# Optimization experiments

Measured on AMD Instinct MI355X. Metric: run time of the kernel, lower is better.

## Reference

```python
import jax, jax.numpy as jnp
import numpy as np
import math

B, I, O, D, H = 32, 1152, 10, 16, 10
SUB = 0.8
S = math.ceil(SUB * I)  # 922 subset size


def _safe_l2norm(x, axis, keepdims=False):
    # L2 norm with zero-safe gradient (forward-identical to jnp.linalg.norm)
    s = jnp.sum(x * x, axis=axis, keepdims=keepdims)
    return jnp.where(s == 0, 0.0, jnp.sqrt(jnp.where(s == 0, 1.0, s)))


def setup_inputs() -> dict:
    key = jax.random.key(0)
    k1, k2 = jax.random.split(key)
    u_predict = jax.random.normal(k1, (B, I, O, D), dtype=jnp.float32)
    # emulate torch.rand(...).topk(S, dim=1).indices: top-S distinct indices along input_caps
    noise = jax.random.uniform(k2, (B, I, O, H))
    sample_idx = jnp.argsort(-noise, axis=1)[:, :S].astype(jnp.int64)  # [B,S,O,H]
    return {"u_predict": u_predict, "sample_idx": sample_idx}


def reference(u_predict, sample_idx):
    b, i, o, d = u_predict.shape
    h = sample_idx.shape[-1]
    # scatter 0/1 hypothesis mask r: [B,I,O,H]
    bi = jnp.arange(b)[:, None, None, None]
    oi = jnp.arange(o)[None, None, :, None]
    hi = jnp.arange(h)[None, None, None, :]
    r = jnp.zeros((b, i, o, h), u_predict.dtype).at[bi, sample_idx, oi, hi].set(1.0)

    # Vr = V_exp * r; since r is 0/1, ||Vr||_D = r * ||V||_D
    Vnorm = _safe_l2norm(u_predict, axis=3)            # [B,I,O]
    Vr_norm = Vnorm[..., None] * r                     # [B,I,O,H]
    # Mu = sum_i(Vr_norm * Vr) / sum_i Vr_norm  (Vr_norm*Vr = r*||V||*V since r^2=r)
    num = jnp.einsum('bioh,biod->bodh', Vr_norm, u_predict)   # [B,O,D,H]
    Mu = num / jnp.sum(Vr_norm, axis=1)[:, :, None, :]        # [B,O,D,H]

    # losses = sum_i ||V_exp - Mu||_D  -> [B,O,H]
    diff = u_predict[..., None] - Mu[:, None]          # [B,I,O,D,H]
    losses = jnp.sum(_safe_l2norm(diff, axis=3), axis=1)
    min_idx = jnp.argmin(losses, axis=2)               # [B,O]

    # pick best hypothesis's mask per (batch, output_caps)
    final_r = jnp.take_along_axis(r, min_idx[:, None, :, None], axis=3)  # [B,I,O,1]

    # capsule weighted average
    u = u_predict * final_r
    un = _safe_l2norm(u, axis=3, keepdims=True)        # [B,I,O,1]
    v = jnp.sum(u * un, axis=1) / jnp.sum(un, axis=1)  # [B,O,D]
    return v
```

## Files before the change

### kernel.cpp

```cpp
#include <hip/hip_runtime.h>
#include <math.h>


#define B_    32
#define I_    1152
#define O_    10
#define D_    16
#define H_    10
#define S_    922
#define COMP  230
#define MASKW 36
#define NT    512
#define NW    8

__device__ __forceinline__ int uoff(int i, int c) {
    return i * 16 + (((c ^ ((i >> 1) & 3)) & 3) << 2);
}

template <int CTRL, int ROWM>
static __device__ __forceinline__ float dpp_f(float v) {
    return __int_as_float(__builtin_amdgcn_update_dpp(
        0, __float_as_int(v), CTRL, ROWM, 0xf, true));
}
static __device__ __forceinline__ float wave_sum_f32(float v) {
    v += dpp_f<0x111, 0xf>(v);
    v += dpp_f<0x112, 0xf>(v);
    v += dpp_f<0x114, 0xf>(v);
    v += dpp_f<0x118, 0xf>(v);
    v += dpp_f<0x142, 0xa>(v);
    v += dpp_f<0x143, 0xc>(v);
    return v;
}
template <int CTRL, int ROWM>
static __device__ __forceinline__ double dpp_d(double v) {
    long long x = __double_as_longlong(v);
    int lo = (int)(unsigned)(x & 0xffffffffLL);
    int hi = (int)(x >> 32);
    lo = __builtin_amdgcn_update_dpp(0, lo, CTRL, ROWM, 0xf, true);
    hi = __builtin_amdgcn_update_dpp(0, hi, CTRL, ROWM, 0xf, true);
    return __longlong_as_double((long long)(unsigned)lo | ((long long)hi << 32));
}
static __device__ __forceinline__ double wave_sum_f64(double v) {
    v += dpp_d<0x111, 0xf>(v);
    v += dpp_d<0x112, 0xf>(v);
    v += dpp_d<0x114, 0xf>(v);
    v += dpp_d<0x118, 0xf>(v);
    v += dpp_d<0x142, 0xa>(v);
    v += dpp_d<0x143, 0xc>(v);
    return v;
}

__global__ __launch_bounds__(NT, 2) void ransac_kernel(
    const float* __restrict__ up,
    const int*   __restrict__ sidx,
    float*       __restrict__ out)
{
    __shared__ float          u_s[I_ * 16];
    __shared__ unsigned       mask[H_][MASKW];
    __shared__ unsigned short clist[H_][COMP];
    __shared__ int            ccount[H_];
    __shared__ float          Mu_s[H_][D_];
    __shared__ float          totred[NW][17];
    __shared__ float          tot[17];
    __shared__ double         lpart[H_][NW];
    __shared__ double         losses[H_];
    __shared__ int            hstar;

    const int blk = blockIdx.x;
    const int xcd = blk & 7, g = blk >> 3;
    const int b   = xcd + 8 * (g / O_);
    const int o   = g - O_ * (g / O_);
    const int bo  = b * O_ + o;

    const int tid  = threadIdx.x;
    const int lane = tid & 63;
    const int wv   = tid >> 6;

    for (int j = tid; j < H_ * MASKW; j += NT) ((unsigned*)mask)[j] = 0u;
    if (tid < H_) ccount[tid] = 0;
    __syncthreads();

    const float* ub = up + ((size_t)b * I_ * O_ + o) * D_;
    float acc[D_]; float accd = 0.f;
    #pragma unroll
    for (int d = 0; d < D_; ++d) acc[d] = 0.f;
    for (int i = tid; i < I_; i += NT) {
        const float4* p = (const float4*)(ub + (size_t)i * (O_ * D_));
        float4 q0 = p[0], q1 = p[1], q2 = p[2], q3 = p[3];
        float s = q0.x*q0.x + q0.y*q0.y + q0.z*q0.z + q0.w*q0.w
                + q1.x*q1.x + q1.y*q1.y + q1.z*q1.z + q1.w*q1.w
                + q2.x*q2.x + q2.y*q2.y + q2.z*q2.z + q2.w*q2.w
                + q3.x*q3.x + q3.y*q3.y + q3.z*q3.z + q3.w*q3.w;
        float vn = sqrtf(s);
        *(float4*)&u_s[uoff(i,0)] = q0;
        *(float4*)&u_s[uoff(i,1)] = q1;
        *(float4*)&u_s[uoff(i,2)] = q2;
        *(float4*)&u_s[uoff(i,3)] = q3;
        acc[ 0] = fmaf(vn, q0.x, acc[ 0]); acc[ 1] = fmaf(vn, q0.y, acc[ 1]);
        acc[ 2] = fmaf(vn, q0.z, acc[ 2]); acc[ 3] = fmaf(vn, q0.w, acc[ 3]);
        acc[ 4] = fmaf(vn, q1.x, acc[ 4]); acc[ 5] = fmaf(vn, q1.y, acc[ 5]);
        acc[ 6] = fmaf(vn, q1.z, acc[ 6]); acc[ 7] = fmaf(vn, q1.w, acc[ 7]);
        acc[ 8] = fmaf(vn, q2.x, acc[ 8]); acc[ 9] = fmaf(vn, q2.y, acc[ 9]);
        acc[10] = fmaf(vn, q2.z, acc[10]); acc[11] = fmaf(vn, q2.w, acc[11]);
        acc[12] = fmaf(vn, q3.x, acc[12]); acc[13] = fmaf(vn, q3.y, acc[13]);
        acc[14] = fmaf(vn, q3.z, acc[14]); acc[15] = fmaf(vn, q3.w, acc[15]);
        accd += vn;
    }

    const int* sb = sidx + (size_t)b * (S_ * O_ * H_) + o * H_;
    for (int j = tid; j < S_ * H_; j += NT) {
        int s = j / H_;
        int h = j - s * H_;
        int idx = sb[s * (O_ * H_) + h];
        atomicOr(&mask[h][idx >> 5], 1u << (idx & 31));
    }

    #pragma unroll
    for (int d = 0; d < D_; ++d) acc[d] = wave_sum_f32(acc[d]);
    accd = wave_sum_f32(accd);
    if (lane == 63) {
        #pragma unroll
        for (int d = 0; d < D_; ++d) totred[wv][d] = acc[d];
        totred[wv][16] = accd;
    }
    __syncthreads();

    if (tid < 17) {
        float t = 0.f;
        #pragma unroll
        for (int w = 0; w < NW; ++w) t += totred[w][tid];
        tot[tid] = t;
    }

    for (int h = wv; h < H_; h += NW) {
        if (lane < MASKW) {
            unsigned m = ~mask[h][lane];
            int cnt = __popc(m);
            int base = atomicAdd(&ccount[h], cnt);
            while (m) {
                int bit = __ffs(m) - 1;
                m &= m - 1u;
                clist[h][base++] = (unsigned short)((lane << 5) + bit);
            }
        }
    }
    __syncthreads();

    for (int h = wv; h < H_; h += NW) {
        float na[D_]; float nd = 0.f;
        #pragma unroll
        for (int d = 0; d < D_; ++d) na[d] = 0.f;
        for (int k = lane; k < COMP; k += 64) {
            int i = clist[h][k];
            float4 q0 = *(const float4*)&u_s[uoff(i,0)];
            float4 q1 = *(const float4*)&u_s[uoff(i,1)];
            float4 q2 = *(const float4*)&u_s[uoff(i,2)];
            float4 q3 = *(const float4*)&u_s[uoff(i,3)];
            float s = q0.x*q0.x + q0.y*q0.y + q0.z*q0.z + q0.w*q0.w
                    + q1.x*q1.x + q1.y*q1.y + q1.z*q1.z + q1.w*q1.w
                    + q2.x*q2.x + q2.y*q2.y + q2.z*q2.z + q2.w*q2.w
                    + q3.x*q3.x + q3.y*q3.y + q3.z*q3.z + q3.w*q3.w;
            float vn = sqrtf(s);
            na[ 0] = fmaf(vn, q0.x, na[ 0]); na[ 1] = fmaf(vn, q0.y, na[ 1]);
            na[ 2] = fmaf(vn, q0.z, na[ 2]); na[ 3] = fmaf(vn, q0.w, na[ 3]);
            na[ 4] = fmaf(vn, q1.x, na[ 4]); na[ 5] = fmaf(vn, q1.y, na[ 5]);
            na[ 6] = fmaf(vn, q1.z, na[ 6]); na[ 7] = fmaf(vn, q1.w, na[ 7]);
            na[ 8] = fmaf(vn, q2.x, na[ 8]); na[ 9] = fmaf(vn, q2.y, na[ 9]);
            na[10] = fmaf(vn, q2.z, na[10]); na[11] = fmaf(vn, q2.w, na[11]);
            na[12] = fmaf(vn, q3.x, na[12]); na[13] = fmaf(vn, q3.y, na[13]);
            na[14] = fmaf(vn, q3.z, na[14]); na[15] = fmaf(vn, q3.w, na[15]);
            nd += vn;
        }
        #pragma unroll
        for (int d = 0; d < D_; ++d) na[d] = wave_sum_f32(na[d]);
        nd = wave_sum_f32(nd);
        if (lane == 63) {
            float rd = 1.f / (tot[16] - nd);
            #pragma unroll
            for (int d = 0; d < D_; ++d)
                Mu_s[h][d] = (tot[d] - na[d]) * rd;
        }
    }
    __syncthreads();

    float mu[H_][D_];
    #pragma unroll
    for (int h = 0; h < H_; ++h) {
        float4 m0 = *(const float4*)&Mu_s[h][0];
        float4 m1 = *(const float4*)&Mu_s[h][4];
        float4 m2 = *(const float4*)&Mu_s[h][8];
        float4 m3 = *(const float4*)&Mu_s[h][12];
        mu[h][ 0]=m0.x; mu[h][ 1]=m0.y; mu[h][ 2]=m0.z; mu[h][ 3]=m0.w;
        mu[h][ 4]=m1.x; mu[h][ 5]=m1.y; mu[h][ 6]=m1.z; mu[h][ 7]=m1.w;
        mu[h][ 8]=m2.x; mu[h][ 9]=m2.y; mu[h][10]=m2.z; mu[h][11]=m2.w;
        mu[h][12]=m3.x; mu[h][13]=m3.y; mu[h][14]=m3.z; mu[h][15]=m3.w;
    }
    float musq[H_];
    #pragma unroll
    for (int h = 0; h < H_; ++h) {
        float s = 0.f;
        #pragma unroll
        for (int d = 0; d < D_; ++d) s = fmaf(mu[h][d], mu[h][d], s);
        musq[h] = s;
    }
    double lacc[H_];
    #pragma unroll
    for (int h = 0; h < H_; ++h) lacc[h] = 0.0;

    auto lossStep = [&](int i) {
        float4 q0 = *(const float4*)&u_s[uoff(i,0)];
        float4 q1 = *(const float4*)&u_s[uoff(i,1)];
        float4 q2 = *(const float4*)&u_s[uoff(i,2)];
        float4 q3 = *(const float4*)&u_s[uoff(i,3)];
        float uq[D_] = {q0.x,q0.y,q0.z,q0.w, q1.x,q1.y,q1.z,q1.w,
                        q2.x,q2.y,q2.z,q2.w, q3.x,q3.y,q3.z,q3.w};
        float usq = 0.f;
        #pragma unroll
        for (int d = 0; d < D_; ++d) usq = fmaf(uq[d], uq[d], usq);
        #pragma unroll
        for (int h = 0; h < H_; ++h) {
            float dot = 0.f;
            #pragma unroll
            for (int d = 0; d < D_; ++d) dot = fmaf(uq[d], mu[h][d], dot);
            float d2 = fmaf(-2.f, dot, usq + musq[h]);
            lacc[h] += (double)sqrtf(fmaxf(d2, 0.f));
        }
    };
    lossStep(tid);
    lossStep(tid + NT);
    if (tid >= 384) lossStep(tid + 640);

    #pragma unroll
    for (int h = 0; h < H_; ++h) lacc[h] = wave_sum_f64(lacc[h]);
    if (lane == 63) {
        #pragma unroll
        for (int h = 0; h < H_; ++h) lpart[h][wv] = lacc[h];
    }
    __syncthreads();

    if (tid < H_) {
        double t = 0.0;
        #pragma unroll
        for (int w = 0; w < NW; ++w) t += lpart[tid][w];
        losses[tid] = t;
    }
    __syncthreads();
    if (tid == 0) {
        int best = 0; double bl = losses[0];
        #pragma unroll
        for (int h = 1; h < H_; ++h)
            if (losses[h] < bl) { bl = losses[h]; best = h; }
        hstar = best;
    }
    __syncthreads();
    if (tid < D_)
        out[(size_t)bo * D_ + tid] = Mu_s[hstar][tid];
}

extern "C" void kernel_launch(void* const* d_in, const int* in_sizes, int n_in,
                              void* d_out, int out_size, void* d_ws, size_t ws_size,
                              hipStream_t stream) {
    const float* up   = (const float*)d_in[0];
    const int*   sidx = (const int*)d_in[1];
    float*       out  = (float*)d_out;
    ransac_kernel<<<B_ * O_, NT, 0, stream>>>(up, sidx, out);
}
```

Baseline: 107.0 us.

## Split fused kernel into mask/mean, per-hypothesis loss, and selection kernels

Replaces the single per-(batch,output) kernel, which staged the capsule slice in LDS, with three launches. The first builds the masks and the per-hypothesis means with one wave per hypothesis, reading complement rows straight from global memory. The second runs one block per (batch, output, hypothesis) to compute the loss and does an atomicMin on a packed loss|index word. The third gathers the winning mean. This spreads the loss work over ten times more blocks to raise occupancy, at the cost of re-reading u_predict from global/L2 up to eleven times, two extra launches, and a small loss-precision truncation in the argmin packing.

```diff
diff --git a/kernel.cpp b/kernel.cpp
--- a/kernel.cpp
+++ b/kernel.cpp
@@ -10,12 +10,6 @@
 #define S_    922
 #define COMP  230
 #define MASKW 36
-#define NT    512
-#define NW    8
-
-__device__ __forceinline__ int uoff(int i, int c) {
-    return i * 16 + (((c ^ ((i >> 1) & 3)) & 3) << 2);
-}
 
 template <int CTRL, int ROWM>
 static __device__ __forceinline__ float dpp_f(float v) {
@@ -50,41 +44,38 @@
     return v;
 }
 
-__global__ __launch_bounds__(NT, 2) void ransac_kernel(
+__global__ __launch_bounds__(640, 1) void k1_mask_mu(
     const float* __restrict__ up,
     const int*   __restrict__ sidx,
-    float*       __restrict__ out)
+    float*       __restrict__ muw,
+    unsigned long long* __restrict__ winner)
 {
-    __shared__ float          u_s[I_ * 16];
     __shared__ unsigned       mask[H_][MASKW];
     __shared__ unsigned short clist[H_][COMP];
     __shared__ int            ccount[H_];
-    __shared__ float          Mu_s[H_][D_];
-    __shared__ float          totred[NW][17];
+    __shared__ float          totred[10][17];
     __shared__ float          tot[17];
-    __shared__ double         lpart[H_][NW];
-    __shared__ double         losses[H_];
-    __shared__ int            hstar;
 
     const int blk = blockIdx.x;
     const int xcd = blk & 7, g = blk >> 3;
     const int b   = xcd + 8 * (g / O_);
-    const int o   = g - O_ * (g / O_);
+    const int o   = g - (g / O_) * O_;
     const int bo  = b * O_ + o;
 
     const int tid  = threadIdx.x;
     const int lane = tid & 63;
     const int wv   = tid >> 6;
 
-    for (int j = tid; j < H_ * MASKW; j += NT) ((unsigned*)mask)[j] = 0u;
+    for (int j = tid; j < H_ * MASKW; j += 640) ((unsigned*)mask)[j] = 0u;
     if (tid < H_) ccount[tid] = 0;
+    if (tid == 0) winner[bo] = ~0ULL;
     __syncthreads();
 
     const float* ub = up + ((size_t)b * I_ * O_ + o) * D_;
-    float acc[D_]; float accd = 0.f;
-    #pragma unroll
-    for (int d = 0; d < D_; ++d) acc[d] = 0.f;
-    for (int i = tid; i < I_; i += NT) {
+    float acc[17];
+    #pragma unroll
+    for (int d = 0; d < 17; ++d) acc[d] = 0.f;
+    for (int i = tid; i < I_; i += 640) {
         const float4* p = (const float4*)(ub + (size_t)i * (O_ * D_));
         float4 q0 = p[0], q1 = p[1], q2 = p[2], q3 = p[3];
         float s = q0.x*q0.x + q0.y*q0.y + q0.z*q0.z + q0.w*q0.w
@@ -92,10 +83,6 @@
                 + q2.x*q2.x + q2.y*q2.y + q2.z*q2.z + q2.w*q2.w
                 + q3.x*q3.x + q3.y*q3.y + q3.z*q3.z + q3.w*q3.w;
         float vn = sqrtf(s);
-        *(float4*)&u_s[uoff(i,0)] = q0;
-        *(float4*)&u_s[uoff(i,1)] = q1;
-        *(float4*)&u_s[uoff(i,2)] = q2;
-        *(float4*)&u_s[uoff(i,3)] = q3;
         acc[ 0] = fmaf(vn, q0.x, acc[ 0]); acc[ 1] = fmaf(vn, q0.y, acc[ 1]);
         acc[ 2] = fmaf(vn, q0.z, acc[ 2]); acc[ 3] = fmaf(vn, q0.w, acc[ 3]);
         acc[ 4] = fmaf(vn, q1.x, acc[ 4]); acc[ 5] = fmaf(vn, q1.y, acc[ 5]);
@@ -104,11 +91,11 @@
         acc[10] = fmaf(vn, q2.z, acc[10]); acc[11] = fmaf(vn, q2.w, acc[11]);
         acc[12] = fmaf(vn, q3.x, acc[12]); acc[13] = fmaf(vn, q3.y, acc[13]);
         acc[14] = fmaf(vn, q3.z, acc[14]); acc[15] = fmaf(vn, q3.w, acc[15]);
-        accd += vn;
+        acc[16] += vn;
     }
 
     const int* sb = sidx + (size_t)b * (S_ * O_ * H_) + o * H_;
-    for (int j = tid; j < S_ * H_; j += NT) {
+    for (int j = tid; j < S_ * H_; j += 640) {
         int s = j / H_;
         int h = j - s * H_;
         int idx = sb[s * (O_ * H_) + h];
@@ -116,46 +103,42 @@
     }
 
     #pragma unroll
-    for (int d = 0; d < D_; ++d) acc[d] = wave_sum_f32(acc[d]);
-    accd = wave_sum_f32(accd);
+    for (int d = 0; d < 17; ++d) acc[d] = wave_sum_f32(acc[d]);
     if (lane == 63) {
         #pragma unroll
-        for (int d = 0; d < D_; ++d) totred[wv][d] = acc[d];
-        totred[wv][16] = accd;
+        for (int d = 0; d < 17; ++d) totred[wv][d] = acc[d];
     }
     __syncthreads();
 
     if (tid < 17) {
         float t = 0.f;
         #pragma unroll
-        for (int w = 0; w < NW; ++w) t += totred[w][tid];
+        for (int w = 0; w < 10; ++w) t += totred[w][tid];
         tot[tid] = t;
     }
 
-    for (int h = wv; h < H_; h += NW) {
-        if (lane < MASKW) {
-            unsigned m = ~mask[h][lane];
-            int cnt = __popc(m);
-            int base = atomicAdd(&ccount[h], cnt);
-            while (m) {
-                int bit = __ffs(m) - 1;
-                m &= m - 1u;
-                clist[h][base++] = (unsigned short)((lane << 5) + bit);
-            }
-        }
-    }
-    __syncthreads();
-
-    for (int h = wv; h < H_; h += NW) {
-        float na[D_]; float nd = 0.f;
-        #pragma unroll
-        for (int d = 0; d < D_; ++d) na[d] = 0.f;
+    if (lane < MASKW) {
+        const int h = wv;
+        unsigned m = ~mask[h][lane];
+        int cnt = __popc(m);
+        int base = atomicAdd(&ccount[h], cnt);
+        while (m) {
+            int bit = __ffs(m) - 1;
+            m &= m - 1u;
+            clist[h][base++] = (unsigned short)((lane << 5) + bit);
+        }
+    }
+    __syncthreads();
+
+    {
+        const int h = wv;
+        float na[17];
+        #pragma unroll
+        for (int d = 0; d < 17; ++d) na[d] = 0.f;
         for (int k = lane; k < COMP; k += 64) {
             int i = clist[h][k];
-            float4 q0 = *(const float4*)&u_s[uoff(i,0)];
-            float4 q1 = *(const float4*)&u_s[uoff(i,1)];
-            float4 q2 = *(const float4*)&u_s[uoff(i,2)];
-            float4 q3 = *(const float4*)&u_s[uoff(i,3)];
+            const float4* p = (const float4*)(ub + (size_t)i * (O_ * D_));
+            float4 q0 = p[0], q1 = p[1], q2 = p[2], q3 = p[3];
             float s = q0.x*q0.x + q0.y*q0.y + q0.z*q0.z + q0.w*q0.w
                     + q1.x*q1.x + q1.y*q1.y + q1.z*q1.z + q1.w*q1.w
                     + q2.x*q2.x + q2.y*q2.y + q2.z*q2.z + q2.w*q2.w
@@ -169,92 +152,87 @@
             na[10] = fmaf(vn, q2.z, na[10]); na[11] = fmaf(vn, q2.w, na[11]);
             na[12] = fmaf(vn, q3.x, na[12]); na[13] = fmaf(vn, q3.y, na[13]);
             na[14] = fmaf(vn, q3.z, na[14]); na[15] = fmaf(vn, q3.w, na[15]);
-            nd += vn;
-        }
-        #pragma unroll
-        for (int d = 0; d < D_; ++d) na[d] = wave_sum_f32(na[d]);
-        nd = wave_sum_f32(nd);
+            na[16] += vn;
+        }
+        #pragma unroll
+        for (int d = 0; d < 17; ++d) na[d] = wave_sum_f32(na[d]);
         if (lane == 63) {
-            float rd = 1.f / (tot[16] - nd);
+            float rd = 1.f / (tot[16] - na[16]);
+            float* mo = muw + ((size_t)bo * H_ + h) * D_;
             #pragma unroll
-            for (int d = 0; d < D_; ++d)
-                Mu_s[h][d] = (tot[d] - na[d]) * rd;
-        }
-    }
-    __syncthreads();
-
-    float mu[H_][D_];
-    #pragma unroll
-    for (int h = 0; h < H_; ++h) {
-        float4 m0 = *(const float4*)&Mu_s[h][0];
-        float4 m1 = *(const float4*)&Mu_s[h][4];
-        float4 m2 = *(const float4*)&Mu_s[h][8];
-        float4 m3 = *(const float4*)&Mu_s[h][12];
-        mu[h][ 0]=m0.x; mu[h][ 1]=m0.y; mu[h][ 2]=m0.z; mu[h][ 3]=m0.w;
-        mu[h][ 4]=m1.x; mu[h][ 5]=m1.y; mu[h][ 6]=m1.z; mu[h][ 7]=m1.w;
-        mu[h][ 8]=m2.x; mu[h][ 9]=m2.y; mu[h][10]=m2.z; mu[h][11]=m2.w;
-        mu[h][12]=m3.x; mu[h][13]=m3.y; mu[h][14]=m3.z; mu[h][15]=m3.w;
-    }
-    float musq[H_];
-    #pragma unroll
-    for (int h = 0; h < H_; ++h) {
-        float s = 0.f;
-        #pragma unroll
-        for (int d = 0; d < D_; ++d) s = fmaf(mu[h][d], mu[h][d], s);
-        musq[h] = s;
-    }
-    double lacc[H_];
-    #pragma unroll
-    for (int h = 0; h < H_; ++h) lacc[h] = 0.0;
-
-    auto lossStep = [&](int i) {
-        float4 q0 = *(const float4*)&u_s[uoff(i,0)];
-        float4 q1 = *(const float4*)&u_s[uoff(i,1)];
-        float4 q2 = *(const float4*)&u_s[uoff(i,2)];
-        float4 q3 = *(const float4*)&u_s[uoff(i,3)];
+            for (int d = 0; d < D_; ++d) mo[d] = (tot[d] - na[d]) * rd;
+        }
+    }
+}
+
+__global__ __launch_bounds__(256, 4) void k2_loss(
+    const float* __restrict__ up,
+    const float* __restrict__ muw,
+    unsigned long long* __restrict__ winner)
+{
+    __shared__ double lpart[4];
+
+    const int g   = blockIdx.x;
+    const int xcd = g & 7;
+    const int r   = g >> 3;
+    const int bhi = r / 100;
+    const int rem = r - 100 * bhi;
+    const int o   = rem / 10;
+    const int h   = rem - 10 * o;
+    const int b   = bhi * 8 + xcd;
+    const int bo  = b * O_ + o;
+
+    const int tid  = threadIdx.x;
+    const int lane = tid & 63;
+    const int wv   = tid >> 6;
+
+    const float* mo = muw + ((size_t)bo * H_ + h) * D_;
+    float mu[D_];
+    #pragma unroll
+    for (int d = 0; d < D_; ++d) mu[d] = mo[d];
+    float musq = 0.f;
+    #pragma unroll
+    for (int d = 0; d < D_; ++d) musq = fmaf(mu[d], mu[d], musq);
+
+    const float* ub = up + ((size_t)b * I_ * O_ + o) * D_;
+    double lacc = 0.0;
+    for (int i = tid; i < I_; i += 256) {
+        const float4* p = (const float4*)(ub + (size_t)i * (O_ * D_));
+        float4 q0 = p[0], q1 = p[1], q2 = p[2], q3 = p[3];
         float uq[D_] = {q0.x,q0.y,q0.z,q0.w, q1.x,q1.y,q1.z,q1.w,
                         q2.x,q2.y,q2.z,q2.w, q3.x,q3.y,q3.z,q3.w};
-        float usq = 0.f;
-        #pragma unroll
-        for (int d = 0; d < D_; ++d) usq = fmaf(uq[d], uq[d], usq);
-        #pragma unroll
-        for (int h = 0; h < H_; ++h) {
-            float dot = 0.f;
-            #pragma unroll
-            for (int d = 0; d < D_; ++d) dot = fmaf(uq[d], mu[h][d], dot);
-            float d2 = fmaf(-2.f, dot, usq + musq[h]);
-            lacc[h] += (double)sqrtf(fmaxf(d2, 0.f));
-        }
-    };
-    lossStep(tid);
-    lossStep(tid + NT);
-    if (tid >= 384) lossStep(tid + 640);
-
-    #pragma unroll
-    for (int h = 0; h < H_; ++h) lacc[h] = wave_sum_f64(lacc[h]);
-    if (lane == 63) {
-        #pragma unroll
-        for (int h = 0; h < H_; ++h) lpart[h][wv] = lacc[h];
-    }
-    __syncthreads();
-
-    if (tid < H_) {
-        double t = 0.0;
-        #pragma unroll
-        for (int w = 0; w < NW; ++w) t += lpart[tid][w];
-        losses[tid] = t;
-    }
+        float usq = 0.f, dot = 0.f;
+        #pragma unroll
+        for (int d = 0; d < D_; ++d) {
+            usq = fmaf(uq[d], uq[d], usq);
+            dot = fmaf(uq[d], mu[d], dot);
+        }
+        float d2 = fmaf(-2.f, dot, usq + musq);
+        lacc += (double)sqrtf(fmaxf(d2, 0.f));
+    }
+    lacc = wave_sum_f64(lacc);
+    if (lane == 63) lpart[wv] = lacc;
     __syncthreads();
     if (tid == 0) {
-        int best = 0; double bl = losses[0];
-        #pragma unroll
-        for (int h = 1; h < H_; ++h)
-            if (losses[h] < bl) { bl = losses[h]; best = h; }
-        hstar = best;
-    }
-    __syncthreads();
-    if (tid < D_)
-        out[(size_t)bo * D_ + tid] = Mu_s[hstar][tid];
+        double L = lpart[0] + lpart[1] + lpart[2] + lpart[3];
+        unsigned long long pk =
+            (((unsigned long long)__double_as_longlong(L)) & ~0xFULL) | (unsigned)h;
+        atomicMin(&winner[bo], pk);
+    }
+}
+
+__global__ __launch_bounds__(256, 4) void k3_out(
+    const float* __restrict__ muw,
+    const unsigned long long* __restrict__ winner,
+    float* __restrict__ out)
+{
+    int g = blockIdx.x * 256 + threadIdx.x;
+    if (g < B_ * O_ * D_) {
+        int bo = g >> 4;
+        int d  = g & 15;
+        int h  = (int)(winner[bo] & 0xF);
+        out[g] = muw[((size_t)bo * H_ + h) * D_ + d];
+    }
 }
 
 extern "C" void kernel_launch(void* const* d_in, const int* in_sizes, int n_in,
@@ -263,5 +241,11 @@
     const float* up   = (const float*)d_in[0];
     const int*   sidx = (const int*)d_in[1];
     float*       out  = (float*)d_out;
-    ransac_kernel<<<B_ * O_, NT, 0, stream>>>(up, sidx, out);
-}
+
+    float* muw = (float*)d_ws;
+    unsigned long long* winner = (unsigned long long*)((char*)d_ws + 204800);
+
+    k1_mask_mu<<<B_ * O_,      640, 0, stream>>>(up, sidx, muw, winner);
+    k2_loss   <<<B_ * O_ * H_, 256, 0, stream>>>(up, muw, winner);
+    k3_out    <<<(B_ * O_ * D_ + 255) / 256, 256, 0, stream>>>(muw, winner, out);
+}
```

Measured after the change: 125.3 us. 17.2% more time.
